# Kernel tuning notes

Measured on AMD Instinct MI355X. Metric: run time of the kernel, lower is better.

The kernel has to match this reference:

```python
import jax, jax.numpy as jnp
import numpy as np

N = 50000
E = 800000
F_IN = 128
HID = 60
CAT = 3 * HID
NUM_CLASSES = 7
EPS = 1e-5


def _gcn_norm(edge_index, n):
    # add self loops, symmetric normalization (PyG gcn_norm default)
    loops = jnp.arange(n, dtype=edge_index.dtype)
    src = jnp.concatenate([edge_index[0], loops])
    dst = jnp.concatenate([edge_index[1], loops])
    deg = jax.ops.segment_sum(jnp.ones_like(src, dtype=jnp.float32), dst, num_segments=n)
    dinv = jnp.where(deg > 0, jax.lax.rsqrt(jnp.maximum(deg, 1.0)), 0.0)
    norm = dinv[src] * dinv[dst]  # [E+N]
    return src, dst, norm


def _prop(x, src, dst, norm, n):
    # sum_{j in N(i)} norm_ij * x_j
    return jax.ops.segment_sum(x[src] * norm[:, None], dst, num_segments=n)


def _mixhop(x, src, dst, norm, n, ws, bs):
    outs = [x @ ws[0] + bs[0]]  # power 0
    h = x
    for w, b in zip(ws[1:], bs[1:]):  # powers 1, 2
        h = _prop(h, src, dst, norm, n)
        outs.append(h @ w + b)
    return jnp.concatenate(outs, axis=-1)


def _batchnorm(x, g, b):
    # training-mode batch stats over node dim (biased variance, eps=1e-5)
    mu = x.mean(axis=0)
    var = x.var(axis=0)
    return (x - mu) * jax.lax.rsqrt(var + EPS) * g + b


def setup_inputs() -> dict:
    key = jax.random.key(0)
    ks = jax.random.split(key, 16)
    x = jax.random.normal(ks[0], (N, F_IN), dtype=jnp.float32)
    edge_index = jax.random.randint(ks[1], (2, E), 0, N, dtype=jnp.int64)
    def lin(k, fi, fo):
        s = 1.0 / np.sqrt(fi)
        return jax.random.uniform(k, (fi, fo), jnp.float32, -s, s)
    inp = {"x": x, "edge_index": edge_index}
    for i, p in enumerate(range(3)):
        inp[f"c1_w{p}"] = lin(ks[2 + p], F_IN, HID)
        inp[f"c1_b{p}"] = jnp.zeros((HID,), jnp.float32)
        inp[f"c2_w{p}"] = lin(ks[5 + p], CAT, HID)
        inp[f"c2_b{p}"] = jnp.zeros((HID,), jnp.float32)
        inp[f"c3_w{p}"] = lin(ks[8 + p], CAT, HID)
        inp[f"c3_b{p}"] = jnp.zeros((HID,), jnp.float32)
    for i in (1, 2, 3):
        inp[f"bn{i}_g"] = jnp.ones((CAT,), jnp.float32)
        inp[f"bn{i}_b"] = jnp.zeros((CAT,), jnp.float32)
    inp["lin_w"] = lin(ks[11], CAT, NUM_CLASSES)
    inp["lin_b"] = jnp.zeros((NUM_CLASSES,), jnp.float32)
    return inp


def reference(x, edge_index,
              c1_w0, c1_b0, c1_w1, c1_b1, c1_w2, c1_b2,
              c2_w0, c2_b0, c2_w1, c2_b1, c2_w2, c2_b2,
              c3_w0, c3_b0, c3_w1, c3_b1, c3_w2, c3_b2,
              bn1_g, bn1_b, bn2_g, bn2_b, bn3_g, bn3_b,
              lin_w, lin_b):
    n = x.shape[0]
    src, dst, norm = _gcn_norm(edge_index, n)
    # dropout layers are identity in eval mode
    h = _mixhop(x, src, dst, norm, n, (c1_w0, c1_w1, c1_w2), (c1_b0, c1_b1, c1_b2))
    h = _batchnorm(h, bn1_g, bn1_b)
    h = _mixhop(h, src, dst, norm, n, (c2_w0, c2_w1, c2_w2), (c2_b0, c2_b1, c2_b2))
    h = _batchnorm(h, bn2_g, bn2_b)
    h = _mixhop(h, src, dst, norm, n, (c3_w0, c3_w1, c3_w2), (c3_b0, c3_b1, c3_b2))
    h = _batchnorm(h, bn3_g, bn3_b)
    return h @ lin_w + lin_b
```

## Files before the change

kernel.cpp:

```cpp
#include <hip/hip_runtime.h>
#include <hip/hip_bf16.h>

#define NN 50000
#define NE 800000
#define FIN0 128
#define HID 60
#define CAT 180
#define NCLS 7
#define BN_EPS 1e-5f
#define NBUCK 196
#define BCAP 5120

typedef unsigned int uint;
typedef unsigned short ushort;
typedef __attribute__((ext_vector_type(8))) short short8;
typedef __attribute__((ext_vector_type(4))) float f32x4;

__device__ __forceinline__ ushort f2bf(float f) {
    uint u = __float_as_uint(f);
    u += 0x7FFFu + ((u >> 16) & 1u);
    return (ushort)(u >> 16);
}
__device__ __forceinline__ float bf_lo(uint v) { return __uint_as_float(v << 16); }
__device__ __forceinline__ float bf_hi(uint v) { return __uint_as_float(v & 0xFFFF0000u); }
__device__ __forceinline__ float bf2f(ushort u) { return __uint_as_float(((uint)u) << 16); }


__global__ void k_initcur(int* __restrict__ gcur) {
    int t = threadIdx.x;
    if (t < NBUCK) gcur[t] = t * BCAP;
}

__global__ __launch_bounds__(256) void k_bin(const int* __restrict__ src,
                                             const int* __restrict__ dst,
                                             int* __restrict__ gcur,
                                             int2* __restrict__ ebuf, int e) {
    __shared__ int cnt[NBUCK];
    __shared__ int base[NBUCK];
    int t = threadIdx.x;
    for (int c0 = blockIdx.x * 2048; c0 < e; c0 += gridDim.x * 2048) {
        if (t < NBUCK) cnt[t] = 0;
        __syncthreads();
        int sv[8], dv[8], rk[8], bk[8], ok[8];
#pragma unroll
        for (int j = 0; j < 8; ++j) {
            int i = c0 + j * 256 + t;
            ok[j] = i < e;
            if (ok[j]) {
                sv[j] = src[i];
                dv[j] = dst[i];
                bk[j] = dv[j] >> 8;
                rk[j] = atomicAdd(&cnt[bk[j]], 1);
            }
        }
        __syncthreads();
        if (t < NBUCK && cnt[t] > 0) base[t] = atomicAdd(&gcur[t], cnt[t]);
        __syncthreads();
#pragma unroll
        for (int j = 0; j < 8; ++j) {
            if (ok[j]) {
                int2 v; v.x = sv[j]; v.y = dv[j];
                ebuf[base[bk[j]] + rk[j]] = v;
            }
        }
        __syncthreads();
    }
}

__global__ void k_bscan(const int* __restrict__ gcur, int* __restrict__ bbase,
                        int* __restrict__ bcnt, int* __restrict__ row_ptr) {
    __shared__ int s[256];
    int t = threadIdx.x;
    int c = (t < NBUCK) ? (gcur[t] - t * BCAP) : 0;
    s[t] = c;
    __syncthreads();
    for (int off = 1; off < 256; off <<= 1) {
        int v = (t >= off) ? s[t - off] : 0;
        __syncthreads();
        s[t] += v;
        __syncthreads();
    }
    if (t < NBUCK) { bbase[t] = s[t] - c; bcnt[t] = c; }
    if (t == 0) row_ptr[NN] = NE;
}

__global__ __launch_bounds__(256) void k_bucket_csr(
        const int2* __restrict__ ebuf, const int* __restrict__ bbase,
        const int* __restrict__ bcnt,
        int* __restrict__ row_ptr, float* __restrict__ dinv,
        int* __restrict__ ssrc, int n) {
    __shared__ int ncnt[256];
    __shared__ int loff[256];
    int b = blockIdx.x, t = threadIdx.x;
    int cnt = bcnt[b];
    int gbase = bbase[b];
    const int2* ee = ebuf + (size_t)b * BCAP;
    ncnt[t] = 0;
    __syncthreads();
    for (int i = t; i < cnt; i += 256) atomicAdd(&ncnt[ee[i].y & 255], 1);
    __syncthreads();
    int c = ncnt[t];
    loff[t] = c;
    __syncthreads();
    for (int off = 1; off < 256; off <<= 1) {
        int v = (t >= off) ? loff[t - off] : 0;
        __syncthreads();
        loff[t] += v;
        __syncthreads();
    }
    int excl = loff[t] - c;
    int node = b * 256 + t;
    if (node < n) {
        row_ptr[node] = gbase + excl;
        dinv[node] = rsqrtf((float)(c + 1));
    }
    __syncthreads();
    ncnt[t] = excl;
    __syncthreads();
    for (int i = t; i < cnt; i += 256) {
        int2 ed = ee[i];
        int pos = atomicAdd(&ncnt[ed.y & 255], 1);
        ssrc[gbase + pos] = ed.x;
    }
}

__global__ __launch_bounds__(256) void k_cast(const float* __restrict__ x,
                                              ushort* __restrict__ xb, size_t total4) {
    size_t stride = (size_t)gridDim.x * blockDim.x;
    for (size_t i = (size_t)blockIdx.x * blockDim.x + threadIdx.x; i < total4; i += stride) {
        float4 v = *(const float4*)(x + i * 4);
        ushort4 o;
        o.x = f2bf(v.x); o.y = f2bf(v.y); o.z = f2bf(v.z); o.w = f2bf(v.w);
        *(ushort4*)(xb + i * 4) = o;
    }
}

__global__ void k_wpack(const float* __restrict__ w0, const float* __restrict__ w1,
                        const float* __restrict__ w2, ushort* __restrict__ WP,
                        int K_real, int KT) {
    int p = blockIdx.y;
    int kt = blockIdx.x >> 2;
    int ct = blockIdx.x & 3;
    const float* __restrict__ W = (p == 0) ? w0 : ((p == 1) ? w1 : w2);
    int lane = threadIdx.x;
    int k0 = kt * 32 + (lane >> 4) * 8;
    int c = ct * 16 + (lane & 15);
    ushort* dst = WP + (((size_t)(p * KT + kt) * 4 + ct) << 9) + (lane << 3);
    ushort4 o0, o1;
    float v;
#define WVAL(J) ((k0 + (J)) < K_real && c < 60) ? W[(size_t)(k0 + (J)) * 60 + c] : 0.f
    v = WVAL(0); o0.x = f2bf(v);
    v = WVAL(1); o0.y = f2bf(v);
    v = WVAL(2); o0.z = f2bf(v);
    v = WVAL(3); o0.w = f2bf(v);
    v = WVAL(4); o1.x = f2bf(v);
    v = WVAL(5); o1.y = f2bf(v);
    v = WVAL(6); o1.z = f2bf(v);
    v = WVAL(7); o1.w = f2bf(v);
#undef WVAL
    *(ushort4*)dst = o0;
    *(ushort4*)(dst + 4) = o1;
}

template <int KT>
__global__ __launch_bounds__(256) void k_gemm_mfma(
        const ushort* __restrict__ XB,
        const ushort* __restrict__ WP,
        const float* __restrict__ b0,
        const float* __restrict__ dinv,
        ushort* __restrict__ Y0,
        ushort* __restrict__ Y12,
        int n) {
    const int t = threadIdx.x;
    const int wv = t >> 6;
    const int lane = t & 63;
    const int l15 = lane & 15;
    const int lhi = lane >> 4;
    const int nb = blockIdx.x * 64 + wv * 16;

    f32x4 acc[3][4];
#pragma unroll
    for (int p = 0; p < 3; ++p)
#pragma unroll
        for (int ct = 0; ct < 4; ++ct) acc[p][ct] = (f32x4){0.f, 0.f, 0.f, 0.f};

    int arow = nb + l15;
    const ushort* xrow = XB + (size_t)(arow < n ? arow : 0) * (KT * 32) + lhi * 8;
    const ushort* wpL = WP + (lane << 3);

#pragma unroll
    for (int kt = 0; kt < KT; ++kt) {
        short8 a = *(const short8*)(xrow + kt * 32);
#pragma unroll
        for (int p = 0; p < 3; ++p)
#pragma unroll
            for (int ct = 0; ct < 4; ++ct) {
                short8 b = *(const short8*)(wpL + (((size_t)(p * KT + kt) * 4 + ct) << 9));
                acc[p][ct] = __builtin_amdgcn_mfma_f32_16x16x32_bf16(a, b, acc[p][ct], 0, 0, 0);
            }
    }

    float dv[4];
#pragma unroll
    for (int j = 0; j < 4; ++j) {
        int node = nb + lhi * 4 + j;
        dv[j] = (node < n) ? dinv[node] : 0.f;
    }
#pragma unroll
    for (int ct = 0; ct < 4; ++ct) {
        int col = ct * 16 + l15;
        if (col >= 60) continue;
        float bias = b0[col];
#pragma unroll
        for (int j = 0; j < 4; ++j) {
            int node = nb + lhi * 4 + j;
            if (node >= n) continue;
            Y0[(size_t)node * 64 + col] = f2bf(acc[0][ct][j] + bias);
            uint pk = ((uint)f2bf(dv[j] * acc[2][ct][j]) << 16) |
                      (uint)f2bf(dv[j] * acc[1][ct][j]);
            *(uint*)(Y12 + (size_t)node * 128 + 2 * col) = pk;
        }
    }
}

__global__ __launch_bounds__(256) void k_propA(
        const ushort* __restrict__ Y12, ushort* __restrict__ Z1, ushort* __restrict__ ZQ,
        const float* __restrict__ b1,
        const float* __restrict__ dinv, const int* __restrict__ rp,
        const int* __restrict__ es, int n) {
    int node = blockIdx.x * 4 + (threadIdx.x >> 6);
    int lane = threadIdx.x & 63;
    if (node >= n || lane >= 60) return;
    uint sv = *(const uint*)(Y12 + (size_t)node * 128 + 2 * lane);
    float a1 = bf_lo(sv);
    float a2 = bf_hi(sv);
    int e0 = rp[node], e1 = rp[node + 1];
    int e = e0;
    for (; e + 7 < e1; e += 8) {
        int s0 = es[e], s1 = es[e + 1], s2 = es[e + 2], s3 = es[e + 3];
        int s4 = es[e + 4], s5 = es[e + 5], s6 = es[e + 6], s7 = es[e + 7];
        uint v0 = *(const uint*)(Y12 + (size_t)s0 * 128 + 2 * lane);
        uint v1 = *(const uint*)(Y12 + (size_t)s1 * 128 + 2 * lane);
        uint v2 = *(const uint*)(Y12 + (size_t)s2 * 128 + 2 * lane);
        uint v3 = *(const uint*)(Y12 + (size_t)s3 * 128 + 2 * lane);
        uint v4 = *(const uint*)(Y12 + (size_t)s4 * 128 + 2 * lane);
        uint v5 = *(const uint*)(Y12 + (size_t)s5 * 128 + 2 * lane);
        uint v6 = *(const uint*)(Y12 + (size_t)s6 * 128 + 2 * lane);
        uint v7 = *(const uint*)(Y12 + (size_t)s7 * 128 + 2 * lane);
        a1 += ((bf_lo(v0) + bf_lo(v1)) + (bf_lo(v2) + bf_lo(v3))) +
              ((bf_lo(v4) + bf_lo(v5)) + (bf_lo(v6) + bf_lo(v7)));
        a2 += ((bf_hi(v0) + bf_hi(v1)) + (bf_hi(v2) + bf_hi(v3))) +
              ((bf_hi(v4) + bf_hi(v5)) + (bf_hi(v6) + bf_hi(v7)));
    }
    for (; e < e1; ++e) {
        uint v = *(const uint*)(Y12 + (size_t)es[e] * 128 + 2 * lane);
        a1 += bf_lo(v);
        a2 += bf_hi(v);
    }
    float di = dinv[node];
    Z1[(size_t)node * 64 + lane] = f2bf(di * a1 + b1[lane]);
    ZQ[(size_t)node * 64 + lane] = f2bf(di * di * a2);
}

__global__ __launch_bounds__(256) void k_propB(
        const ushort* __restrict__ ZQ, ushort* __restrict__ Q2,
        const float* __restrict__ b2,
        const float* __restrict__ dinv, const int* __restrict__ rp,
        const int* __restrict__ es, int n) {
    int node = blockIdx.x * 4 + (threadIdx.x >> 6);
    int lane = threadIdx.x & 63;
    if (node >= n || lane >= 60) return;
    float acc = bf2f(ZQ[(size_t)node * 64 + lane]);
    int e0 = rp[node], e1 = rp[node + 1];
    int e = e0;
    for (; e + 7 < e1; e += 8) {
        int s0 = es[e], s1 = es[e + 1], s2 = es[e + 2], s3 = es[e + 3];
        int s4 = es[e + 4], s5 = es[e + 5], s6 = es[e + 6], s7 = es[e + 7];
        float x0 = bf2f(ZQ[(size_t)s0 * 64 + lane]);
        float x1 = bf2f(ZQ[(size_t)s1 * 64 + lane]);
        float x2 = bf2f(ZQ[(size_t)s2 * 64 + lane]);
        float x3 = bf2f(ZQ[(size_t)s3 * 64 + lane]);
        float x4 = bf2f(ZQ[(size_t)s4 * 64 + lane]);
        float x5 = bf2f(ZQ[(size_t)s5 * 64 + lane]);
        float x6 = bf2f(ZQ[(size_t)s6 * 64 + lane]);
        float x7 = bf2f(ZQ[(size_t)s7 * 64 + lane]);
        acc += ((x0 + x1) + (x2 + x3)) + ((x4 + x5) + (x6 + x7));
    }
    for (; e < e1; ++e) {
        acc += bf2f(ZQ[(size_t)es[e] * 64 + lane]);
    }
    Q2[(size_t)node * 64 + lane] = f2bf(dinv[node] * acc + b2[lane]);
}

__global__ __launch_bounds__(256) void k_bnstats(
        const ushort* __restrict__ Y0, const ushort* __restrict__ Z1,
        const ushort* __restrict__ Q2,
        float* __restrict__ gsum, float* __restrict__ gsum2, int n) {
    int rgn = blockIdx.y;
    const ushort* __restrict__ src = (rgn == 0) ? Y0 : ((rgn == 1) ? Z1 : Q2);
    int t = threadIdx.x;
    int c8 = (t & 7) * 8;
    int rsub = t >> 3;
    float s1[8], s2[8];
#pragma unroll
    for (int j = 0; j < 8; ++j) { s1[j] = 0.f; s2[j] = 0.f; }
    for (int r = blockIdx.x * 32 + rsub; r < n; r += gridDim.x * 32) {
        uint4 v = *(const uint4*)(src + (size_t)r * 64 + c8);
        float f;
        f = bf_lo(v.x); s1[0] += f; s2[0] += f * f;
        f = bf_hi(v.x); s1[1] += f; s2[1] += f * f;
        f = bf_lo(v.y); s1[2] += f; s2[2] += f * f;
        f = bf_hi(v.y); s1[3] += f; s2[3] += f * f;
        f = bf_lo(v.z); s1[4] += f; s2[4] += f * f;
        f = bf_hi(v.z); s1[5] += f; s2[5] += f * f;
        f = bf_lo(v.w); s1[6] += f; s2[6] += f * f;
        f = bf_hi(v.w); s1[7] += f; s2[7] += f * f;
    }
#pragma unroll
    for (int m = 8; m < 64; m <<= 1) {
#pragma unroll
        for (int j = 0; j < 8; ++j) {
            s1[j] += __shfl_xor(s1[j], m);
            s2[j] += __shfl_xor(s2[j], m);
        }
    }
    __shared__ float ls1[4][64], ls2[4][64];
    int wv = t >> 6, lane = t & 63;
    if (lane < 8) {
#pragma unroll
        for (int j = 0; j < 8; ++j) {
            ls1[wv][lane * 8 + j] = s1[j];
            ls2[wv][lane * 8 + j] = s2[j];
        }
    }
    __syncthreads();
    if (t < 64 && t < 60) {
        float a1 = ls1[0][t] + ls1[1][t] + ls1[2][t] + ls1[3][t];
        float a2 = ls2[0][t] + ls2[1][t] + ls2[2][t] + ls2[3][t];
        atomicAdd(&gsum[rgn * 60 + t], a1);
        atomicAdd(&gsum2[rgn * 60 + t], a2);
    }
}

__global__ __launch_bounds__(256) void k_bnapply(
        const ushort* __restrict__ Y0, const ushort* __restrict__ Z1,
        const ushort* __restrict__ Q2,
        const float* __restrict__ gsum, const float* __restrict__ gsum2,
        const float* __restrict__ g, const float* __restrict__ b,
        ushort* __restrict__ CB, int n, size_t total) {
    __shared__ float ssc[CAT], ssh[CAT];
    int tt = threadIdx.x;
    if (tt < CAT) {
        float mu = gsum[tt] / (float)n;
        float var = gsum2[tt] / (float)n - mu * mu;
        float sc = rsqrtf(var + BN_EPS) * g[tt];
        ssc[tt] = sc;
        ssh[tt] = b[tt] - mu * sc;
    }
    __syncthreads();
    size_t stride = (size_t)gridDim.x * blockDim.x;
    for (size_t i = (size_t)blockIdx.x * blockDim.x + tt; i < total; i += stride) {
        size_t node = i / 48;
        int c0 = (int)(i % 48) * 4;
        ushort4 o;
        if (c0 >= CAT) {
            o.x = 0; o.y = 0; o.z = 0; o.w = 0;
        } else {
            const ushort* sp;
            if (c0 < 60) sp = Y0 + node * 64 + c0;
            else if (c0 < 120) sp = Z1 + node * 64 + (c0 - 60);
            else sp = Q2 + node * 64 + (c0 - 120);
            uint u0 = *(const uint*)sp;
            uint u1 = *(const uint*)(sp + 2);
            o.x = f2bf(bf_lo(u0) * ssc[c0 + 0] + ssh[c0 + 0]);
            o.y = f2bf(bf_hi(u0) * ssc[c0 + 1] + ssh[c0 + 1]);
            o.z = f2bf(bf_lo(u1) * ssc[c0 + 2] + ssh[c0 + 2]);
            o.w = f2bf(bf_hi(u1) * ssc[c0 + 3] + ssh[c0 + 3]);
        }
        *(ushort4*)(CB + node * 192 + c0) = o;
    }
}

__global__ __launch_bounds__(256) void k_final_fused(
        const ushort* __restrict__ Y0, const ushort* __restrict__ Z1,
        const ushort* __restrict__ Q2,
        const float* __restrict__ gsum, const float* __restrict__ gsum2,
        const float* __restrict__ g, const float* __restrict__ bb,
        const float* __restrict__ w, const float* __restrict__ wb,
        float* __restrict__ out, int n) {
    __shared__ float sw[CAT * NCLS];
    __shared__ float ssc[CAT], ssh[CAT];
    __shared__ float sb[NCLS];
    int t = threadIdx.x;
    for (int i = t; i < CAT * NCLS; i += 256) sw[i] = w[i];
    if (t < CAT) {
        float mu = gsum[t] / (float)n;
        float var = gsum2[t] / (float)n - mu * mu;
        float sc = rsqrtf(var + BN_EPS) * g[t];
        ssc[t] = sc;
        ssh[t] = bb[t] - mu * sc;
    }
    if (t < NCLS) sb[t] = wb[t];
    __syncthreads();
    int node = blockIdx.x * 256 + t;
    if (node >= n) return;
    float acc[NCLS];
#pragma unroll
    for (int j = 0; j < NCLS; ++j) acc[j] = sb[j];
    const ushort* bufs[3] = {Y0, Z1, Q2};
#pragma unroll
    for (int rgn = 0; rgn < 3; ++rgn) {
        const ushort* sp = bufs[rgn] + (size_t)node * 64;
        int cb = rgn * 60;
#pragma unroll 6
        for (int k2 = 0; k2 < 30; ++k2) {
            uint u = *(const uint*)(sp + 2 * k2);
            int c = cb + 2 * k2;
            float f0 = bf_lo(u) * ssc[c] + ssh[c];
            float f1 = bf_hi(u) * ssc[c + 1] + ssh[c + 1];
#pragma unroll
            for (int j = 0; j < NCLS; ++j)
                acc[j] += f0 * sw[c * NCLS + j] + f1 * sw[(c + 1) * NCLS + j];
        }
    }
#pragma unroll
    for (int j = 0; j < NCLS; ++j) out[(size_t)node * NCLS + j] = acc[j];
}

extern "C" void kernel_launch(void* const* d_in, const int* in_sizes, int n_in,
                              void* d_out, int out_size, void* d_ws, size_t ws_size,
                              hipStream_t stream) {
    const float* x = (const float*)d_in[0];
    const int* ei = (const int*)d_in[1];
    const int* esrc = ei;
    const int* edst = ei + NE;

    const float* c_w[3][3];
    const float* c_b[3][3];
    for (int p = 0; p < 3; ++p)
        for (int l = 0; l < 3; ++l) {
            c_w[l][p] = (const float*)d_in[2 + p * 6 + l * 2];
            c_b[l][p] = (const float*)d_in[3 + p * 6 + l * 2];
        }
    const float* bn_g[3] = {(const float*)d_in[20], (const float*)d_in[22], (const float*)d_in[24]};
    const float* bn_b[3] = {(const float*)d_in[21], (const float*)d_in[23], (const float*)d_in[25]};
    const float* lw = (const float*)d_in[26];
    const float* lb = (const float*)d_in[27];
    float* out = (float*)d_out;

    char* wp = (char*)d_ws;
    auto alloc = [&](size_t bytes) {
        char* p = wp;
        wp += (bytes + 255) & ~(size_t)255;
        return p;
    };
    int* gcur = (int*)alloc((size_t)NBUCK * 4);
    int* bbase = (int*)alloc((size_t)(NBUCK + 1) * 4);
    int* bcnt = (int*)alloc((size_t)NBUCK * 4);
    int2* ebuf = (int2*)alloc((size_t)NBUCK * BCAP * 8);
    int* row_ptr = (int*)alloc((size_t)(NN + 1) * 4);
    int* ssrc = (int*)alloc((size_t)NE * 4);
    float* dinv = (float*)alloc((size_t)NN * 4);
    float* gsum = (float*)alloc((size_t)2 * CAT * 4);
    float* gsum2 = gsum + CAT;
    ushort* Y0 = (ushort*)alloc((size_t)NN * 64 * 2);
    ushort* Y12 = (ushort*)alloc((size_t)NN * 128 * 2);
    ushort* Z1 = (ushort*)alloc((size_t)NN * 64 * 2);
    ushort* ZQ = (ushort*)alloc((size_t)NN * 64 * 2);
    ushort* Q2 = (ushort*)alloc((size_t)NN * 64 * 2);
    ushort* XB1 = (ushort*)alloc((size_t)NN * 128 * 2);
    ushort* CB = (ushort*)alloc((size_t)NN * 192 * 2);
    ushort* WP1 = (ushort*)alloc((size_t)3 * 4 * 4 * 512 * 2);
    ushort* WP2 = (ushort*)alloc((size_t)3 * 6 * 4 * 512 * 2);
    ushort* WP3 = (ushort*)alloc((size_t)3 * 6 * 4 * 512 * 2);

    k_initcur<<<1, 256, 0, stream>>>(gcur);
    k_bin<<<391, 256, 0, stream>>>(esrc, edst, gcur, ebuf, NE);
    k_bscan<<<1, 256, 0, stream>>>(gcur, bbase, bcnt, row_ptr);
    k_bucket_csr<<<NBUCK, 256, 0, stream>>>(ebuf, bbase, bcnt, row_ptr, dinv, ssrc, NN);

    k_cast<<<2048, 256, 0, stream>>>(x, XB1, (size_t)NN * 128 / 4);
    k_wpack<<<dim3(16, 3), 64, 0, stream>>>(c_w[0][0], c_w[0][1], c_w[0][2], WP1, FIN0, 4);
    k_wpack<<<dim3(24, 3), 64, 0, stream>>>(c_w[1][0], c_w[1][1], c_w[1][2], WP2, CAT, 6);
    k_wpack<<<dim3(24, 3), 64, 0, stream>>>(c_w[2][0], c_w[2][1], c_w[2][2], WP3, CAT, 6);

    const int gemm_gx = (NN + 63) / 64;
    const int prop_gx = (NN + 3) / 4;
    const size_t bn_total = (size_t)NN * 48;

    for (int l = 0; l < 3; ++l) {
        if (l == 0) {
            k_gemm_mfma<4><<<gemm_gx, 256, 0, stream>>>(XB1, WP1, c_b[0][0], dinv, Y0, Y12, NN);
        } else {
            const ushort* WPl = (l == 1) ? WP2 : WP3;
            k_gemm_mfma<6><<<gemm_gx, 256, 0, stream>>>(CB, WPl, c_b[l][0], dinv, Y0, Y12, NN);
        }
        k_propA<<<prop_gx, 256, 0, stream>>>(Y12, Z1, ZQ, c_b[l][1], dinv, row_ptr, ssrc, NN);
        k_propB<<<prop_gx, 256, 0, stream>>>(ZQ, Q2, c_b[l][2], dinv, row_ptr, ssrc, NN);
        hipMemsetAsync(gsum, 0, (size_t)2 * CAT * 4, stream);
        k_bnstats<<<dim3(256, 3), 256, 0, stream>>>(Y0, Z1, Q2, gsum, gsum2, NN);
        if (l < 2) {
            k_bnapply<<<2048, 256, 0, stream>>>(Y0, Z1, Q2, gsum, gsum2, bn_g[l], bn_b[l],
                                                CB, NN, bn_total);
        } else {
            k_final_fused<<<(NN + 255) / 256, 256, 0, stream>>>(
                Y0, Z1, Q2, gsum, gsum2, bn_g[2], bn_b[2], lw, lb, out, NN);
        }
    }
}
```

Baseline: 398.1 us.

## Fuse BN apply and input cast into GEMM, compress edge indices to 16-bit

Batch-norm scale/shift is now applied inside the GEMM's A-operand load, reading Y0/Z1/Q2 directly. This removes the separate bnapply pass and its concatenated CB buffer. Layer 1 converts fp32 x to bf16 inside the GEMM instead of running a cast kernel. Edge binning packs source (16 bits) and local destination into one 32-bit word, and the CSR source array is stored as ushort, cutting index traffic in binning and in both propagation kernels. The three weight-pack launches become one, and BN-stat buffers are cleared with a single memset; this relies on the node count fitting in 16 bits and on the GEMM reading and writing Y0 in place.

```diff
diff --git a/kernel.cpp b/kernel.cpp
--- a/kernel.cpp
+++ b/kernel.cpp
@@ -34,22 +34,22 @@
 __global__ __launch_bounds__(256) void k_bin(const int* __restrict__ src,
                                              const int* __restrict__ dst,
                                              int* __restrict__ gcur,
-                                             int2* __restrict__ ebuf, int e) {
+                                             uint* __restrict__ ebuf, int e) {
     __shared__ int cnt[NBUCK];
     __shared__ int base[NBUCK];
     int t = threadIdx.x;
     for (int c0 = blockIdx.x * 2048; c0 < e; c0 += gridDim.x * 2048) {
         if (t < NBUCK) cnt[t] = 0;
         __syncthreads();
-        int sv[8], dv[8], rk[8], bk[8], ok[8];
+        uint pe[8]; int rk[8], bk[8], ok[8];
 #pragma unroll
         for (int j = 0; j < 8; ++j) {
             int i = c0 + j * 256 + t;
             ok[j] = i < e;
             if (ok[j]) {
-                sv[j] = src[i];
-                dv[j] = dst[i];
-                bk[j] = dv[j] >> 8;
+                int sv = src[i], dv = dst[i];
+                pe[j] = (uint)(sv & 0xFFFF) | ((uint)(dv & 255) << 16);
+                bk[j] = dv >> 8;
                 rk[j] = atomicAdd(&cnt[bk[j]], 1);
             }
         }
@@ -58,10 +58,7 @@
         __syncthreads();
 #pragma unroll
         for (int j = 0; j < 8; ++j) {
-            if (ok[j]) {
-                int2 v; v.x = sv[j]; v.y = dv[j];
-                ebuf[base[bk[j]] + rk[j]] = v;
-            }
+            if (ok[j]) ebuf[base[bk[j]] + rk[j]] = pe[j];
         }
         __syncthreads();
     }
@@ -85,19 +82,19 @@
 }
 
 __global__ __launch_bounds__(256) void k_bucket_csr(
-        const int2* __restrict__ ebuf, const int* __restrict__ bbase,
+        const uint* __restrict__ ebuf, const int* __restrict__ bbase,
         const int* __restrict__ bcnt,
         int* __restrict__ row_ptr, float* __restrict__ dinv,
-        int* __restrict__ ssrc, int n) {
+        ushort* __restrict__ ssrc, int n) {
     __shared__ int ncnt[256];
     __shared__ int loff[256];
     int b = blockIdx.x, t = threadIdx.x;
     int cnt = bcnt[b];
     int gbase = bbase[b];
-    const int2* ee = ebuf + (size_t)b * BCAP;
+    const uint* ee = ebuf + (size_t)b * BCAP;
     ncnt[t] = 0;
     __syncthreads();
-    for (int i = t; i < cnt; i += 256) atomicAdd(&ncnt[ee[i].y & 255], 1);
+    for (int i = t; i < cnt; i += 256) atomicAdd(&ncnt[(ee[i] >> 16) & 255], 1);
     __syncthreads();
     int c = ncnt[t];
     loff[t] = c;
@@ -118,60 +115,76 @@
     ncnt[t] = excl;
     __syncthreads();
     for (int i = t; i < cnt; i += 256) {
-        int2 ed = ee[i];
-        int pos = atomicAdd(&ncnt[ed.y & 255], 1);
-        ssrc[gbase + pos] = ed.x;
-    }
-}
-
-__global__ __launch_bounds__(256) void k_cast(const float* __restrict__ x,
-                                              ushort* __restrict__ xb, size_t total4) {
-    size_t stride = (size_t)gridDim.x * blockDim.x;
-    for (size_t i = (size_t)blockIdx.x * blockDim.x + threadIdx.x; i < total4; i += stride) {
-        float4 v = *(const float4*)(x + i * 4);
-        ushort4 o;
-        o.x = f2bf(v.x); o.y = f2bf(v.y); o.z = f2bf(v.z); o.w = f2bf(v.w);
-        *(ushort4*)(xb + i * 4) = o;
-    }
-}
-
-__global__ void k_wpack(const float* __restrict__ w0, const float* __restrict__ w1,
-                        const float* __restrict__ w2, ushort* __restrict__ WP,
-                        int K_real, int KT) {
-    int p = blockIdx.y;
-    int kt = blockIdx.x >> 2;
-    int ct = blockIdx.x & 3;
-    const float* __restrict__ W = (p == 0) ? w0 : ((p == 1) ? w1 : w2);
+        uint pe = ee[i];
+        int pos = atomicAdd(&ncnt[(pe >> 16) & 255], 1);
+        ssrc[gbase + pos] = (ushort)(pe & 0xFFFF);
+    }
+}
+
+__global__ void k_wpack_all(
+        const float* __restrict__ w00, const float* __restrict__ w01, const float* __restrict__ w02,
+        const float* __restrict__ w10, const float* __restrict__ w11, const float* __restrict__ w12,
+        const float* __restrict__ w20, const float* __restrict__ w21, const float* __restrict__ w22,
+        ushort* __restrict__ WP0, ushort* __restrict__ WP1, ushort* __restrict__ WP2) {
+    int l = blockIdx.z, p = blockIdx.y;
+    int kt = blockIdx.x >> 2, ct = blockIdx.x & 3;
+    int KT = (l == 0) ? 4 : 6;
+    if (kt >= KT) return;
+    const float* W;
+    if (l == 0) W = (p == 0) ? w00 : ((p == 1) ? w01 : w02);
+    else if (l == 1) W = (p == 0) ? w10 : ((p == 1) ? w11 : w12);
+    else W = (p == 0) ? w20 : ((p == 1) ? w21 : w22);
+    ushort* WP = (l == 0) ? WP0 : ((l == 1) ? WP1 : WP2);
     int lane = threadIdx.x;
     int k0 = kt * 32 + (lane >> 4) * 8;
     int c = ct * 16 + (lane & 15);
     ushort* dst = WP + (((size_t)(p * KT + kt) * 4 + ct) << 9) + (lane << 3);
-    ushort4 o0, o1;
-    float v;
-#define WVAL(J) ((k0 + (J)) < K_real && c < 60) ? W[(size_t)(k0 + (J)) * 60 + c] : 0.f
-    v = WVAL(0); o0.x = f2bf(v);
-    v = WVAL(1); o0.y = f2bf(v);
-    v = WVAL(2); o0.z = f2bf(v);
-    v = WVAL(3); o0.w = f2bf(v);
-    v = WVAL(4); o1.x = f2bf(v);
-    v = WVAL(5); o1.y = f2bf(v);
-    v = WVAL(6); o1.z = f2bf(v);
-    v = WVAL(7); o1.w = f2bf(v);
-#undef WVAL
-    *(ushort4*)dst = o0;
-    *(ushort4*)(dst + 4) = o1;
-}
-
-template <int KT>
+    ushort o[8];
+#pragma unroll
+    for (int j = 0; j < 8; ++j) {
+        int kl = k0 + j;
+        float v = 0.f;
+        if (c < 60) {
+            if (l == 0) {
+                if (kl < FIN0) v = W[(size_t)kl * 60 + c];
+            } else {
+                int rgn = kl >> 6, cc = kl & 63;
+                if (cc < 60) v = W[(size_t)(rgn * 60 + cc) * 60 + c];
+            }
+        }
+        o[j] = f2bf(v);
+    }
+    *(ushort4*)dst = make_ushort4(o[0], o[1], o[2], o[3]);
+    *(ushort4*)(dst + 4) = make_ushort4(o[4], o[5], o[6], o[7]);
+}
+
+template <int KT, int MODE>
 __global__ __launch_bounds__(256) void k_gemm_mfma(
-        const ushort* __restrict__ XB,
+        const float* __restrict__ Xf,
+        const ushort* __restrict__ B0q, const ushort* __restrict__ B1q,
+        const ushort* __restrict__ B2q,
+        const float* __restrict__ gsum, const float* __restrict__ gsum2,
+        const float* __restrict__ bng, const float* __restrict__ bnb,
         const ushort* __restrict__ WP,
-        const float* __restrict__ b0,
-        const float* __restrict__ dinv,
-        ushort* __restrict__ Y0,
-        ushort* __restrict__ Y12,
-        int n) {
+        const float* __restrict__ b0, const float* __restrict__ dinv,
+        ushort* __restrict__ Y0, ushort* __restrict__ Y12, int n) {
+    __shared__ float ssc[200], ssh[200];
     const int t = threadIdx.x;
+    if (MODE == 1) {
+        if (t < 192) {
+            int rgn = t >> 6, cc = t & 63;
+            float sc = 0.f, sh = 0.f;
+            if (cc < 60) {
+                int c = rgn * 60 + cc;
+                float mu = gsum[c] / (float)n;
+                float var = gsum2[c] / (float)n - mu * mu;
+                sc = rsqrtf(var + BN_EPS) * bng[c];
+                sh = bnb[c] - mu * sc;
+            }
+            ssc[t] = sc; ssh[t] = sh;
+        }
+        __syncthreads();
+    }
     const int wv = t >> 6;
     const int lane = t & 63;
     const int l15 = lane & 15;
@@ -184,13 +197,39 @@
 #pragma unroll
         for (int ct = 0; ct < 4; ++ct) acc[p][ct] = (f32x4){0.f, 0.f, 0.f, 0.f};
 
-    int arow = nb + l15;
-    const ushort* xrow = XB + (size_t)(arow < n ? arow : 0) * (KT * 32) + lhi * 8;
+    const int arow = nb + l15;
+    const int arowc = (arow < n) ? arow : 0;
     const ushort* wpL = WP + (lane << 3);
 
 #pragma unroll
     for (int kt = 0; kt < KT; ++kt) {
-        short8 a = *(const short8*)(xrow + kt * 32);
+        short8 a;
+        if (MODE == 0) {
+            const float* xr = Xf + (size_t)arowc * (KT * 32) + kt * 32 + lhi * 8;
+            float4 v0 = *(const float4*)xr;
+            float4 v1 = *(const float4*)(xr + 4);
+            a[0] = (short)f2bf(v0.x); a[1] = (short)f2bf(v0.y);
+            a[2] = (short)f2bf(v0.z); a[3] = (short)f2bf(v0.w);
+            a[4] = (short)f2bf(v1.x); a[5] = (short)f2bf(v1.y);
+            a[6] = (short)f2bf(v1.z); a[7] = (short)f2bf(v1.w);
+        } else {
+            const ushort* base = (kt < 2) ? B0q : ((kt < 4) ? B1q : B2q);
+            const ushort* ar = base + (size_t)arowc * 64 + (kt & 1) * 32 + lhi * 8;
+            uint4 raw = *(const uint4*)ar;
+            int kb = kt * 32 + lhi * 8;
+            float4 sc0 = *(const float4*)&ssc[kb];
+            float4 sc1 = *(const float4*)&ssc[kb + 4];
+            float4 sh0 = *(const float4*)&ssh[kb];
+            float4 sh1 = *(const float4*)&ssh[kb + 4];
+            a[0] = (short)f2bf(bf_lo(raw.x) * sc0.x + sh0.x);
+            a[1] = (short)f2bf(bf_hi(raw.x) * sc0.y + sh0.y);
+            a[2] = (short)f2bf(bf_lo(raw.y) * sc0.z + sh0.z);
+            a[3] = (short)f2bf(bf_hi(raw.y) * sc0.w + sh0.w);
+            a[4] = (short)f2bf(bf_lo(raw.z) * sc1.x + sh1.x);
+            a[5] = (short)f2bf(bf_hi(raw.z) * sc1.y + sh1.y);
+            a[6] = (short)f2bf(bf_lo(raw.w) * sc1.z + sh1.z);
+            a[7] = (short)f2bf(bf_hi(raw.w) * sc1.w + sh1.w);
+        }
 #pragma unroll
         for (int p = 0; p < 3; ++p)
 #pragma unroll
@@ -227,7 +266,7 @@
         const ushort* __restrict__ Y12, ushort* __restrict__ Z1, ushort* __restrict__ ZQ,
         const float* __restrict__ b1,
         const float* __restrict__ dinv, const int* __restrict__ rp,
-        const int* __restrict__ es, int n) {
+        const ushort* __restrict__ es, int n) {
     int node = blockIdx.x * 4 + (threadIdx.x >> 6);
     int lane = threadIdx.x & 63;
     if (node >= n || lane >= 60) return;
@@ -266,7 +305,7 @@
         const ushort* __restrict__ ZQ, ushort* __restrict__ Q2,
         const float* __restrict__ b2,
         const float* __restrict__ dinv, const int* __restrict__ rp,
-        const int* __restrict__ es, int n) {
+        const ushort* __restrict__ es, int n) {
     int node = blockIdx.x * 4 + (threadIdx.x >> 6);
     int lane = threadIdx.x & 63;
     if (node >= n || lane >= 60) return;
@@ -334,50 +373,11 @@
         }
     }
     __syncthreads();
-    if (t < 64 && t < 60) {
+    if (t < 60) {
         float a1 = ls1[0][t] + ls1[1][t] + ls1[2][t] + ls1[3][t];
         float a2 = ls2[0][t] + ls2[1][t] + ls2[2][t] + ls2[3][t];
         atomicAdd(&gsum[rgn * 60 + t], a1);
         atomicAdd(&gsum2[rgn * 60 + t], a2);
-    }
-}
-
-__global__ __launch_bounds__(256) void k_bnapply(
-        const ushort* __restrict__ Y0, const ushort* __restrict__ Z1,
-        const ushort* __restrict__ Q2,
-        const float* __restrict__ gsum, const float* __restrict__ gsum2,
-        const float* __restrict__ g, const float* __restrict__ b,
-        ushort* __restrict__ CB, int n, size_t total) {
-    __shared__ float ssc[CAT], ssh[CAT];
-    int tt = threadIdx.x;
-    if (tt < CAT) {
-        float mu = gsum[tt] / (float)n;
-        float var = gsum2[tt] / (float)n - mu * mu;
-        float sc = rsqrtf(var + BN_EPS) * g[tt];
-        ssc[tt] = sc;
-        ssh[tt] = b[tt] - mu * sc;
-    }
-    __syncthreads();
-    size_t stride = (size_t)gridDim.x * blockDim.x;
-    for (size_t i = (size_t)blockIdx.x * blockDim.x + tt; i < total; i += stride) {
-        size_t node = i / 48;
-        int c0 = (int)(i % 48) * 4;
-        ushort4 o;
-        if (c0 >= CAT) {
-            o.x = 0; o.y = 0; o.z = 0; o.w = 0;
-        } else {
-            const ushort* sp;
-            if (c0 < 60) sp = Y0 + node * 64 + c0;
-            else if (c0 < 120) sp = Z1 + node * 64 + (c0 - 60);
-            else sp = Q2 + node * 64 + (c0 - 120);
-            uint u0 = *(const uint*)sp;
-            uint u1 = *(const uint*)(sp + 2);
-            o.x = f2bf(bf_lo(u0) * ssc[c0 + 0] + ssh[c0 + 0]);
-            o.y = f2bf(bf_hi(u0) * ssc[c0 + 1] + ssh[c0 + 1]);
-            o.z = f2bf(bf_lo(u1) * ssc[c0 + 2] + ssh[c0 + 2]);
-            o.w = f2bf(bf_hi(u1) * ssc[c0 + 3] + ssh[c0 + 3]);
-        }
-        *(ushort4*)(CB + node * 192 + c0) = o;
     }
 }
 
@@ -457,54 +457,54 @@
     int* gcur = (int*)alloc((size_t)NBUCK * 4);
     int* bbase = (int*)alloc((size_t)(NBUCK + 1) * 4);
     int* bcnt = (int*)alloc((size_t)NBUCK * 4);
-    int2* ebuf = (int2*)alloc((size_t)NBUCK * BCAP * 8);
+    uint* ebuf = (uint*)alloc((size_t)NBUCK * BCAP * 4);
     int* row_ptr = (int*)alloc((size_t)(NN + 1) * 4);
-    int* ssrc = (int*)alloc((size_t)NE * 4);
+    ushort* ssrc = (ushort*)alloc((size_t)NE * 2);
     float* dinv = (float*)alloc((size_t)NN * 4);
-    float* gsum = (float*)alloc((size_t)2 * CAT * 4);
-    float* gsum2 = gsum + CAT;
+    float* gsumAll = (float*)alloc((size_t)3 * 2 * CAT * 4);
     ushort* Y0 = (ushort*)alloc((size_t)NN * 64 * 2);
     ushort* Y12 = (ushort*)alloc((size_t)NN * 128 * 2);
     ushort* Z1 = (ushort*)alloc((size_t)NN * 64 * 2);
     ushort* ZQ = (ushort*)alloc((size_t)NN * 64 * 2);
     ushort* Q2 = (ushort*)alloc((size_t)NN * 64 * 2);
-    ushort* XB1 = (ushort*)alloc((size_t)NN * 128 * 2);
-    ushort* CB = (ushort*)alloc((size_t)NN * 192 * 2);
     ushort* WP1 = (ushort*)alloc((size_t)3 * 4 * 4 * 512 * 2);
     ushort* WP2 = (ushort*)alloc((size_t)3 * 6 * 4 * 512 * 2);
     ushort* WP3 = (ushort*)alloc((size_t)3 * 6 * 4 * 512 * 2);
+
+    auto gs = [&](int l) { return gsumAll + (size_t)l * 2 * CAT; };
+    auto gs2 = [&](int l) { return gsumAll + (size_t)l * 2 * CAT + CAT; };
 
     k_initcur<<<1, 256, 0, stream>>>(gcur);
     k_bin<<<391, 256, 0, stream>>>(esrc, edst, gcur, ebuf, NE);
     k_bscan<<<1, 256, 0, stream>>>(gcur, bbase, bcnt, row_ptr);
     k_bucket_csr<<<NBUCK, 256, 0, stream>>>(ebuf, bbase, bcnt, row_ptr, dinv, ssrc, NN);
 
-    k_cast<<<2048, 256, 0, stream>>>(x, XB1, (size_t)NN * 128 / 4);
-    k_wpack<<<dim3(16, 3), 64, 0, stream>>>(c_w[0][0], c_w[0][1], c_w[0][2], WP1, FIN0, 4);
-    k_wpack<<<dim3(24, 3), 64, 0, stream>>>(c_w[1][0], c_w[1][1], c_w[1][2], WP2, CAT, 6);
-    k_wpack<<<dim3(24, 3), 64, 0, stream>>>(c_w[2][0], c_w[2][1], c_w[2][2], WP3, CAT, 6);
+    k_wpack_all<<<dim3(24, 3, 3), 64, 0, stream>>>(
+        c_w[0][0], c_w[0][1], c_w[0][2],
+        c_w[1][0], c_w[1][1], c_w[1][2],
+        c_w[2][0], c_w[2][1], c_w[2][2],
+        WP1, WP2, WP3);
+    hipMemsetAsync(gsumAll, 0, (size_t)3 * 2 * CAT * 4, stream);
 
     const int gemm_gx = (NN + 63) / 64;
     const int prop_gx = (NN + 3) / 4;
-    const size_t bn_total = (size_t)NN * 48;
 
     for (int l = 0; l < 3; ++l) {
         if (l == 0) {
-            k_gemm_mfma<4><<<gemm_gx, 256, 0, stream>>>(XB1, WP1, c_b[0][0], dinv, Y0, Y12, NN);
+            k_gemm_mfma<4, 0><<<gemm_gx, 256, 0, stream>>>(
+                x, nullptr, nullptr, nullptr, nullptr, nullptr, nullptr, nullptr,
+                WP1, c_b[0][0], dinv, Y0, Y12, NN);
         } else {
             const ushort* WPl = (l == 1) ? WP2 : WP3;
-            k_gemm_mfma<6><<<gemm_gx, 256, 0, stream>>>(CB, WPl, c_b[l][0], dinv, Y0, Y12, NN);
+            k_gemm_mfma<6, 1><<<gemm_gx, 256, 0, stream>>>(
+                nullptr, Y0, Z1, Q2, gs(l - 1), gs2(l - 1), bn_g[l - 1], bn_b[l - 1],
+                WPl, c_b[l][0], dinv, Y0, Y12, NN);
         }
         k_propA<<<prop_gx, 256, 0, stream>>>(Y12, Z1, ZQ, c_b[l][1], dinv, row_ptr, ssrc, NN);
         k_propB<<<prop_gx, 256, 0, stream>>>(ZQ, Q2, c_b[l][2], dinv, row_ptr, ssrc, NN);
-        hipMemsetAsync(gsum, 0, (size_t)2 * CAT * 4, stream);
-        k_bnstats<<<dim3(256, 3), 256, 0, stream>>>(Y0, Z1, Q2, gsum, gsum2, NN);
-        if (l < 2) {
-            k_bnapply<<<2048, 256, 0, stream>>>(Y0, Z1, Q2, gsum, gsum2, bn_g[l], bn_b[l],
-                                                CB, NN, bn_total);
-        } else {
-            k_final_fused<<<(NN + 255) / 256, 256, 0, stream>>>(
-                Y0, Z1, Q2, gsum, gsum2, bn_g[2], bn_b[2], lw, lb, out, NN);
-        }
-    }
-}
+        k_bnstats<<<dim3(256, 3), 256, 0, stream>>>(Y0, Z1, Q2, gs(l), gs2(l), NN);
+    }
+
+    k_final_fused<<<(NN + 255) / 256, 256, 0, stream>>>(
+        Y0, Z1, Q2, gs(2), gs2(2), bn_g[2], bn_b[2], lw, lb, out, NN);
+}
```

New measurement: 383.1 us. 1.04x faster.
